# Performance work log

Hardware: AMD Instinct MI355X
Metric: run time of the kernel (lower is better)

## Reference

```python
import jax, jax.numpy as jnp
import numpy as np


def _gru_step(h, x, Wih, Whh, bih, bhh):
    # PyTorch GRU gate order: reset, update, new
    H = h.shape[-1]
    gx = x @ Wih.T + bih            # [B, 3H]
    gh = h @ Whh.T + bhh            # [B, 3H]
    r = jax.nn.sigmoid(gx[:, :H] + gh[:, :H])
    z = jax.nn.sigmoid(gx[:, H:2 * H] + gh[:, H:2 * H])
    n = jnp.tanh(gx[:, 2 * H:] + r * gh[:, 2 * H:])
    return (1.0 - z) * n + z * h


def setup_inputs() -> dict:
    key = jax.random.key(0)
    ks = jax.random.split(key, 20)
    B, S, L = 32, 200, 50
    Vt, Vs = 50000, 30000
    De, Ds, H = 256, 256, 512
    s = 0.05
    f = jnp.float32
    return {
        "method_code": jax.random.randint(ks[0], (B, S), 0, Vt),
        "method_summary": jax.random.randint(ks[1], (B, L), 0, Vs),
        "use_teacher": 1,
        "enc_emb": jax.random.normal(ks[2], (Vt, De), f) * s,
        "enc_Wih": jax.random.normal(ks[3], (3 * H, De), f) * s,
        "enc_Whh": jax.random.normal(ks[4], (3 * H, H), f) * s,
        "enc_bih": jax.random.normal(ks[5], (3 * H,), f) * s,
        "enc_bhh": jax.random.normal(ks[6], (3 * H,), f) * s,
        "dec_emb": jax.random.normal(ks[7], (Vs, Ds), f) * s,
        "dec_Wih": jax.random.normal(ks[8], (3 * H, Ds), f) * s,
        "dec_Whh": jax.random.normal(ks[9], (3 * H, H), f) * s,
        "dec_bih": jax.random.normal(ks[10], (3 * H,), f) * s,
        "dec_bhh": jax.random.normal(ks[11], (3 * H,), f) * s,
        "W1": jax.random.normal(ks[12], (H, 2 * H), f) * s,
        "b1": jax.random.normal(ks[13], (H,), f) * s,
        "W2": jax.random.normal(ks[14], (Vs, H), f) * s,
        "b2": jax.random.normal(ks[15], (Vs,), f) * s,
    }


def reference(method_code, method_summary, use_teacher,
              enc_emb, enc_Wih, enc_Whh, enc_bih, enc_bhh,
              dec_emb, dec_Wih, dec_Whh, dec_bih, dec_bhh,
              W1, b1, W2, b2):
    B = method_code.shape[0]
    H = enc_Whh.shape[1]
    # ---- GRU encoder over code tokens (hidden=None -> zeros) ----
    x_emb = enc_emb[method_code]                       # [B, S, De]
    h0 = jnp.zeros((B, H), x_emb.dtype)

    def enc_step(h, x):
        h = _gru_step(h, x, enc_Wih, enc_Whh, enc_bih, enc_bhh)
        return h, h

    h_last, enc_seq = jax.lax.scan(enc_step, h0, jnp.swapaxes(x_emb, 0, 1))
    enc_out = jnp.swapaxes(enc_seq, 0, 1)              # [B, S, H]

    # ---- attentive GRU decoder, teacher forcing (use_teacher=True) ----
    tokens = method_summary[:, :-1].T                  # [L-1, B]

    def dec_step(h, tok):
        emb = dec_emb[tok]                             # [B, Ds]
        h = _gru_step(h, emb, dec_Wih, dec_Whh, dec_bih, dec_bhh)
        attn = jax.nn.softmax(jnp.einsum('bh,bsh->bs', h, enc_out), axis=-1)
        ctx = jnp.einsum('bs,bsh->bh', attn, enc_out)  # [B, H]
        c = jnp.concatenate([ctx, h], axis=-1)         # [B, 2H]
        out = jax.nn.relu(c @ W1.T + b1) @ W2.T + b2   # [B, Vs]
        return h, out

    _, outs = jax.lax.scan(dec_step, h_last, tokens)   # [L-1, B, Vs]
    return jnp.swapaxes(outs, 0, 1)                    # [B, L-1, Vs]
```

## Files before the change

### kernel.cpp

```cpp
#include <hip/hip_runtime.h>
#include <cmath>

#define WGS  256
#define NWGR 256
#define DOMS 4
#define JGN  64
#define HBDW 5120

typedef float    f32x4 __attribute__((ext_vector_type(4)));
typedef unsigned u32x4 __attribute__((ext_vector_type(4)));
typedef short    s16x8 __attribute__((ext_vector_type(8)));
typedef unsigned short u16x4 __attribute__((ext_vector_type(4)));

#define B_   32
#define S_   200
#define L_   50
#define H_   512
#define DE_  256
#define VS_  30000
#define TD_  49
#define G3_  1536

#define OFF_ENC_GX  ((size_t)0)
#define SZ_ENC_GX   ((size_t)S_*B_*G3_)
#define OFF_DEC_GX  (OFF_ENC_GX + SZ_ENC_GX)
#define SZ_DEC_GX   ((size_t)TD_*B_*G3_)
#define OFF_ENC_OUT (OFF_DEC_GX + SZ_DEC_GX)
#define SZ_ENC_OUT  ((size_t)B_*S_*H_)
#define OFF_HBUF    (OFF_ENC_OUT + SZ_ENC_OUT)
#define SZ_HBUF     ((size_t)DOMS*2*HBDW)
#define OFF_CMAT    (OFF_HBUF + SZ_HBUF)
#define SZ_CMAT     ((size_t)TD_*B_*2*H_)
#define OFF_OUT1    (OFF_CMAT + SZ_CMAT)
#define SZ_OUT1     ((size_t)TD_*B_*H_)
#define OFF_W2HI    ((size_t)0)
#define OFF_W2LO    ((size_t)(VS_*H_/2))
#define OFF_O1HI    (OFF_OUT1 + SZ_OUT1)
#define OFF_O1LO    (OFF_O1HI + (size_t)(TD_*B_*H_/2))

#define RSTR 548
#define KBLK 68

__device__ __forceinline__ u32x4 load_u4_cc(const unsigned* p) {
  u32x4 v;
  asm volatile("global_load_dwordx4 %0, %1, off sc0 sc1" : "=v"(v) : "v"(p) : "memory");
  return v;
}

__device__ __forceinline__ float dot4(f32x4 a, f32x4 b) {
  return a.x * b.x + a.y * b.y + a.z * b.z + a.w * b.w;
}

__device__ __forceinline__ unsigned short f2bf(float f) {
  unsigned u = __float_as_uint(f);
  return (unsigned short)((u + 0x7fffu + ((u >> 16) & 1u)) >> 16);
}
__device__ __forceinline__ float bf2f(unsigned short h) {
  return __uint_as_float(((unsigned)h) << 16);
}

__global__ __launch_bounds__(WGS)
void recurrence_kernel(const float* __restrict__ enc_gx,
                       const float* __restrict__ dec_gx,
                       const float* __restrict__ eWhh, const float* __restrict__ eBhh,
                       const float* __restrict__ dWhh, const float* __restrict__ dBhh,
                       float* __restrict__ enc_out,
                       float* __restrict__ hbuf,
                       float* __restrict__ Cmat)
{
  __shared__ float hlds[8 * RSTR];
  __shared__ float red[768];

  const int t   = threadIdx.x;
  const int w   = blockIdx.x;
  const int dom = w >> 6;
  const int jg  = w & (JGN - 1);
  const int jl  = t & 7;
  const int kh  = t >> 3;
  const int bt_ = t >> 3;
  const int j   = (jg << 3) + jl;
  const int b_g = (dom << 3) + bt_;

  float* hdom = hbuf + (size_t)dom * (2 * HBDW);

  int rr[5], kb[5];
  #pragma unroll
  for (int i = 0; i < 5; ++i) {
    int g = i * 1024 + (t << 2);
    int blk = g / 80;
    rr[i] = g - blk * 80;
    kb[i] = blk << 3;
  }

  f32x4 wreg[3][4];
  auto load_w = [&](const float* __restrict__ W) {
    #pragma unroll
    for (int g = 0; g < 3; ++g)
      #pragma unroll
      for (int c = 0; c < 4; ++c)
        wreg[g][c] = *(const f32x4*)(W + (size_t)(g * H_ + j) * H_ + (kh << 4) + (c << 2));
  };
  load_w(eWhh);

  float bias_r = 0.f, bias_z = 0.f, bias_n = 0.f;
  if (t < 64) { bias_r = eBhh[j]; bias_z = eBhh[H_ + j]; bias_n = eBhh[2 * H_ + j]; }

  for (int s = 0; s < S_ + TD_; ++s) {
    const bool enc = (s < S_);
    __syncthreads();
    if (s == S_) {
      load_w(dWhh);
      if (t < 64) { bias_r = dBhh[j]; bias_z = dBhh[H_ + j]; bias_n = dBhh[2 * H_ + j]; }
    }

    float gxr = 0.f, gxz = 0.f, gxn = 0.f;
    if (t < 64) {
      const float* gx = enc ? (enc_gx + ((size_t)s * B_ + b_g) * G3_)
                            : (dec_gx + ((size_t)(s - S_) * B_ + b_g) * G3_);
      gxr = gx[j]; gxz = gx[H_ + j]; gxn = gx[2 * H_ + j];
    }

    {
      const unsigned* hb = (const unsigned*)(hdom + (size_t)(s & 1) * HBDW);
      const unsigned tagreq = (unsigned)s;
      u32x4 v0, v1, v2, v3, v4;
      while (true) {
        v0 = load_u4_cc(hb + 0 * 1024 + (t << 2));
        v1 = load_u4_cc(hb + 1 * 1024 + (t << 2));
        v2 = load_u4_cc(hb + 2 * 1024 + (t << 2));
        v3 = load_u4_cc(hb + 3 * 1024 + (t << 2));
        v4 = load_u4_cc(hb + 4 * 1024 + (t << 2));
        asm volatile("s_waitcnt vmcnt(0)" ::: "memory");
        bool ok = true;
        if ((rr[0] & 15) == 0) ok &= ((unsigned)v0.x >= tagreq);
        if ((rr[1] & 15) == 0) ok &= ((unsigned)v1.x >= tagreq);
        if ((rr[2] & 15) == 0) ok &= ((unsigned)v2.x >= tagreq);
        if ((rr[3] & 15) == 0) ok &= ((unsigned)v3.x >= tagreq);
        if ((rr[4] & 15) == 0) ok &= ((unsigned)v4.x >= tagreq);
        if (__all(ok)) break;
        __builtin_amdgcn_s_sleep(1);
      }
      #define SCAT(vv, ii) { \
        _Pragma("unroll") \
        for (int d = 0; d < 4; ++d) { \
          int pos = rr[ii] + d; \
          if ((pos & 15) != 0) { \
            int p = pos - 1 - (pos >> 4); \
            if (p < 64) { \
              int bb = p >> 3, k = kb[ii] + (p & 7); \
              hlds[bb * RSTR + ((k >> 6) * KBLK) + (k & 63)] = __uint_as_float(vv[d]); \
            } } } }
      SCAT(v0, 0) SCAT(v1, 1) SCAT(v2, 2) SCAT(v3, 3) SCAT(v4, 4)
      #undef SCAT
    }
    __syncthreads();

    float acc[3][8];
    #pragma unroll
    for (int g = 0; g < 3; ++g)
      #pragma unroll
      for (int b = 0; b < 8; ++b) acc[g][b] = 0.f;

    const int hoff = (kh >> 2) * KBLK + ((kh & 3) << 4);
    #pragma unroll
    for (int b = 0; b < 8; ++b) {
      const float* hp = &hlds[b * RSTR + hoff];
      f32x4 h0 = *(const f32x4*)(hp);
      f32x4 h1 = *(const f32x4*)(hp + 4);
      f32x4 h2 = *(const f32x4*)(hp + 8);
      f32x4 h3 = *(const f32x4*)(hp + 12);
      #pragma unroll
      for (int g = 0; g < 3; ++g)
        acc[g][b] += dot4(wreg[g][0], h0) + dot4(wreg[g][1], h1)
                   + dot4(wreg[g][2], h2) + dot4(wreg[g][3], h3);
    }

    #pragma unroll
    for (int g = 0; g < 3; ++g)
      #pragma unroll
      for (int b = 0; b < 8; ++b) {
        float v = acc[g][b];
        v += __shfl_xor(v, 8);
        v += __shfl_xor(v, 16);
        v += __shfl_xor(v, 32);
        acc[g][b] = v;
      }
    if ((t & 56) == 0) {
      const int base = ((t >> 6) * 8 + jl) * 24;
      #pragma unroll
      for (int g = 0; g < 3; ++g)
        #pragma unroll
        for (int b = 0; b < 8; ++b)
          red[base + g * 8 + b] = acc[g][b];
    }
    __syncthreads();

    if (t < 64) {
      float ar = 0.f, az = 0.f, an = 0.f;
      #pragma unroll
      for (int ww = 0; ww < 4; ++ww) {
        const int base = (ww * 8 + jl) * 24;
        ar += red[base + bt_];
        az += red[base + 8 + bt_];
        an += red[base + 16 + bt_];
      }
      float rg = 1.f / (1.f + expf(-(gxr + ar + bias_r)));
      float zg = 1.f / (1.f + expf(-(gxz + az + bias_z)));
      float ng = tanhf(gxn + rg * (an + bias_n));
      float hprev = hlds[bt_ * RSTR + ((j >> 6) * KBLK) + (j & 63)];
      float hn = (1.f - zg) * ng + zg * hprev;
      if (enc) enc_out[((size_t)b_g * S_ + s) * H_ + j] = hn;
      else     Cmat[((size_t)(s - S_) * B_ + b_g) * (2 * H_) + H_ + j] = hn;

      unsigned* pb = (unsigned*)(hdom + (size_t)((s + 1) & 1) * HBDW) + jg * 80;
      const unsigned tagv = (unsigned)(s + 1);
      float vA = __shfl(hn, (t - 1 - (t >> 4)) & 63);
      unsigned valA = ((t & 15) == 0) ? tagv : __float_as_uint(vA);
      __hip_atomic_store(pb + t, valA, __ATOMIC_RELAXED, __HIP_MEMORY_SCOPE_AGENT);
      float vB = __shfl(hn, (59 + t) & 63);
      if (t < 16) {
        unsigned valB = (t == 0) ? tagv : __float_as_uint(vB);
        __hip_atomic_store(pb + 64 + t, valB, __ATOMIC_RELAXED, __HIP_MEMORY_SCOPE_AGENT);
      }
    }
  }
}

__global__ __launch_bounds__(WGS)
void attention_kernel(const float* __restrict__ enc_out,
                      float* __restrict__ Cmat)
{
  const int task = blockIdx.x;
  const int td = task >> 5, b = task & 31;
  const int t = threadIdx.x;
  const float* h = Cmat + ((size_t)td * B_ + b) * (2 * H_) + H_;

  __shared__ float red[WGS];
  __shared__ float p[WGS];

  float sv = -1e30f;
  if (t < S_) {
    const float* eo = enc_out + ((size_t)b * S_ + t) * H_;
    float acc = 0.f;
    #pragma unroll 4
    for (int k = 0; k < H_; k += 4) {
      float4 e = *(const float4*)(eo + k);
      float4 hv = *(const float4*)(h + k);
      acc += e.x * hv.x + e.y * hv.y + e.z * hv.z + e.w * hv.w;
    }
    sv = acc;
  }
  red[t] = sv; __syncthreads();
  for (int o = 128; o; o >>= 1) { if (t < o) red[t] = fmaxf(red[t], red[t + o]); __syncthreads(); }
  float mx = red[0]; __syncthreads();
  float ev = (t < S_) ? expf(sv - mx) : 0.f;
  red[t] = ev; __syncthreads();
  for (int o = 128; o; o >>= 1) { if (t < o) red[t] += red[t + o]; __syncthreads(); }
  float inv = 1.f / red[0];
  p[t] = ev * inv;
  __syncthreads();

  const float* eo = enc_out + (size_t)b * S_ * H_ + (t << 1);
  float ax = 0.f, ay = 0.f;
  for (int i = 0; i < S_; ++i) {
    float pi = p[i];
    float2 v = *(const float2*)(eo + (size_t)i * H_);
    ax += pi * v.x; ay += pi * v.y;
  }
  float* cd = Cmat + ((size_t)td * B_ + b) * (2 * H_) + (t << 1);
  cd[0] = ax; cd[1] = ay;
}

template<int MODE>
__launch_bounds__(WGS)
__global__ void gemm128g(const float* __restrict__ A,
                         const int* __restrict__ idx,
                         const float* __restrict__ Bw,
                         const float* __restrict__ bias,
                         float* __restrict__ Cdst,
                         unsigned short* __restrict__ Ohi,
                         unsigned short* __restrict__ Olo,
                         int M, int N, int K)
{
  const int APAD = 132;
  __shared__ float As[16 * APAD];
  __shared__ float Bs[16 * APAD];
  __shared__ int toks[128];
  const int n0 = blockIdx.x * 128, m0 = blockIdx.y * 128;
  const int t = threadIdx.x;
  const int tx = t & 15, ty = t >> 4;

  if (MODE <= 1) {
    if (t < 128) {
      int m = m0 + t;
      int tok = 0;
      if (m < M) {
        int bidx = m & 31, sr = m >> 5;
        tok = (MODE == 0) ? idx[bidx * S_ + sr] : idx[bidx * L_ + sr];
      }
      toks[t] = tok;
    }
    __syncthreads();
  }

  float acc[8][8];
  #pragma unroll
  for (int i = 0; i < 8; ++i)
    #pragma unroll
    for (int jj = 0; jj < 8; ++jj) acc[i][jj] = 0.f;

  const int srow = t >> 2, skk = (t & 3) * 4;
  for (int k0 = 0; k0 < K; k0 += 16) {
    #pragma unroll
    for (int u = 0; u < 2; ++u) {
      int row = srow + u * 64;
      const float* asrc;
      if (MODE <= 1) {
        asrc = A + (size_t)toks[row] * K + k0 + skk;
      } else {
        int m = m0 + row; if (m >= M) m = M - 1;
        asrc = A + (size_t)m * K + k0 + skk;
      }
      f32x4 av = *(const f32x4*)asrc;
      As[(skk + 0) * APAD + row] = av.x;
      As[(skk + 1) * APAD + row] = av.y;
      As[(skk + 2) * APAD + row] = av.z;
      As[(skk + 3) * APAD + row] = av.w;
      int n = n0 + row;
      f32x4 bv = *(const f32x4*)(Bw + (size_t)n * K + k0 + skk);
      Bs[(skk + 0) * APAD + row] = bv.x;
      Bs[(skk + 1) * APAD + row] = bv.y;
      Bs[(skk + 2) * APAD + row] = bv.z;
      Bs[(skk + 3) * APAD + row] = bv.w;
    }
    __syncthreads();
    #pragma unroll
    for (int k = 0; k < 16; ++k) {
      f32x4 a0 = *(const f32x4*)&As[k * APAD + ty * 8];
      f32x4 a1 = *(const f32x4*)&As[k * APAD + ty * 8 + 4];
      f32x4 b0 = *(const f32x4*)&Bs[k * APAD + tx * 4];
      f32x4 b1 = *(const f32x4*)&Bs[k * APAD + 64 + tx * 4];
      float a[8] = {a0.x, a0.y, a0.z, a0.w, a1.x, a1.y, a1.z, a1.w};
      float bb[8] = {b0.x, b0.y, b0.z, b0.w, b1.x, b1.y, b1.z, b1.w};
      #pragma unroll
      for (int i = 0; i < 8; ++i)
        #pragma unroll
        for (int jj = 0; jj < 8; ++jj)
          acc[i][jj] += a[i] * bb[jj];
    }
    __syncthreads();
  }

  if (MODE <= 1) {
    f32x4 bias0 = *(const f32x4*)(bias + n0 + tx * 4);
    f32x4 bias1 = *(const f32x4*)(bias + n0 + 64 + tx * 4);
    #pragma unroll
    for (int i = 0; i < 8; ++i) {
      int m = m0 + ty * 8 + i;
      if (m >= M) continue;
      float* orow = Cdst + (size_t)m * N;
      f32x4 v0 = { acc[i][0] + bias0.x, acc[i][1] + bias0.y,
                   acc[i][2] + bias0.z, acc[i][3] + bias0.w };
      f32x4 v1 = { acc[i][4] + bias1.x, acc[i][5] + bias1.y,
                   acc[i][6] + bias1.z, acc[i][7] + bias1.w };
      *(f32x4*)(orow + n0 + tx * 4) = v0;
      *(f32x4*)(orow + n0 + 64 + tx * 4) = v1;
    }
  } else {
    #pragma unroll
    for (int i = 0; i < 8; ++i) {
      int m = m0 + ty * 8 + i;
      if (m >= M) continue;
      #pragma unroll
      for (int half = 0; half < 2; ++half) {
        u16x4 hv, lv;
        #pragma unroll
        for (int d = 0; d < 4; ++d) {
          int n = n0 + half * 64 + tx * 4 + d;
          float v = fmaxf(acc[i][half * 4 + d] + bias[n], 0.f);
          unsigned short hb = f2bf(v);
          hv[d] = hb;
          lv[d] = f2bf(v - bf2f(hb));
        }
        size_t o = (size_t)m * H_ + n0 + half * 64 + tx * 4;
        *(u16x4*)(Ohi + o) = hv;
        *(u16x4*)(Olo + o) = lv;
      }
    }
  }
}

__global__ __launch_bounds__(WGS)
void cvt_split(const float* __restrict__ x, unsigned short* __restrict__ hi,
               unsigned short* __restrict__ lo, int n4)
{
  int i = blockIdx.x * WGS + threadIdx.x;
  if (i >= n4) return;
  f32x4 v = *(const f32x4*)(x + (size_t)i * 4);
  u16x4 h, l;
  #pragma unroll
  for (int d = 0; d < 4; ++d) {
    unsigned short hb = f2bf(v[d]);
    h[d] = hb;
    l[d] = f2bf(v[d] - bf2f(hb));
  }
  *(u16x4*)(hi + (size_t)i * 4) = h;
  *(u16x4*)(lo + (size_t)i * 4) = l;
}

__global__ __launch_bounds__(WGS)
void gemm_mfma_out(const unsigned short* __restrict__ Ahi,
                   const unsigned short* __restrict__ Alo,
                   const unsigned short* __restrict__ Bhi,
                   const unsigned short* __restrict__ Blo,
                   const float* __restrict__ bias,
                   float* __restrict__ out)
{
  __shared__ char smem[65536];
  const int t = threadIdx.x;
  const int l = t & 63;
  const int wv = t >> 6;
  const int r = l & 15, q = l >> 4;
  const int m0 = blockIdx.x * 128;
  const int n0 = blockIdx.y * 128;
  const int M = TD_ * B_, N = VS_, K = H_;
  const int wm = (wv >> 1) << 6;
  const int wn = (wv & 1) << 6;

  int swoff[2];
  size_t aoff[2], boff[2];
  #pragma unroll
  for (int qq = 0; qq < 2; ++qq) {
    int chunk = qq * 256 + t;
    int row = chunk >> 2, c = chunk & 3;
    swoff[qq] = row * 64 + ((c ^ ((row >> 1) & 3)) << 4);
    int gm = m0 + row; if (gm >= M) gm = M - 1;
    aoff[qq] = (size_t)gm * K + c * 8;
    int gn = n0 + row; if (gn >= N) gn = N - 1;
    boff[qq] = (size_t)gn * K + c * 8;
  }

  u32x4 rg[8];
  auto gload = [&](int k0) {
    #pragma unroll
    for (int qq = 0; qq < 2; ++qq) {
      rg[qq]     = *(const u32x4*)(Ahi + aoff[qq] + k0);
      rg[2 + qq] = *(const u32x4*)(Alo + aoff[qq] + k0);
      rg[4 + qq] = *(const u32x4*)(Bhi + boff[qq] + k0);
      rg[6 + qq] = *(const u32x4*)(Blo + boff[qq] + k0);
    }
  };
  auto swrite = [&](char* buf) {
    #pragma unroll
    for (int qq = 0; qq < 2; ++qq) {
      *(u32x4*)(buf +         swoff[qq]) = rg[qq];
      *(u32x4*)(buf +  8192 + swoff[qq]) = rg[2 + qq];
      *(u32x4*)(buf + 16384 + swoff[qq]) = rg[4 + qq];
      *(u32x4*)(buf + 24576 + swoff[qq]) = rg[6 + qq];
    }
  };

  int afo[4], bfo[4];
  #pragma unroll
  for (int fi = 0; fi < 4; ++fi) {
    int ra = wm + fi * 16 + r;
    afo[fi] = ra * 64 + ((q ^ ((ra >> 1) & 3)) << 4);
    int rb = wn + fi * 16 + r;
    bfo[fi] = rb * 64 + ((q ^ ((rb >> 1) & 3)) << 4);
  }

  f32x4 acc[4][4];
  #pragma unroll
  for (int fi = 0; fi < 4; ++fi)
    #pragma unroll
    for (int nj = 0; nj < 4; ++nj) acc[fi][nj] = (f32x4){0.f, 0.f, 0.f, 0.f};

  gload(0);
  swrite(smem);
  __syncthreads();
  int cur = 0;
  const int NS = K / 32;
  for (int s = 0; s < NS; ++s) {
    if (s + 1 < NS) gload((s + 1) * 32);
    char* buf = smem + cur * 32768;
    s16x8 ah[4], al[4], bh[4], bl[4];
    #pragma unroll
    for (int fi = 0; fi < 4; ++fi) {
      ah[fi] = *(const s16x8*)(buf +         afo[fi]);
      al[fi] = *(const s16x8*)(buf +  8192 + afo[fi]);
      bh[fi] = *(const s16x8*)(buf + 16384 + bfo[fi]);
      bl[fi] = *(const s16x8*)(buf + 24576 + bfo[fi]);
    }
    #pragma unroll
    for (int fi = 0; fi < 4; ++fi)
      #pragma unroll
      for (int nj = 0; nj < 4; ++nj) {
        acc[fi][nj] = __builtin_amdgcn_mfma_f32_16x16x32_bf16(ah[fi], bh[nj], acc[fi][nj], 0, 0, 0);
        acc[fi][nj] = __builtin_amdgcn_mfma_f32_16x16x32_bf16(ah[fi], bl[nj], acc[fi][nj], 0, 0, 0);
        acc[fi][nj] = __builtin_amdgcn_mfma_f32_16x16x32_bf16(al[fi], bh[nj], acc[fi][nj], 0, 0, 0);
      }
    if (s + 1 < NS) swrite(smem + (cur ^ 1) * 32768);
    __syncthreads();
    cur ^= 1;
  }

  #pragma unroll
  for (int nj = 0; nj < 4; ++nj) {
    int n = n0 + wn + nj * 16 + r;
    if (n >= N) continue;
    float bv = bias[n];
    #pragma unroll
    for (int fi = 0; fi < 4; ++fi) {
      #pragma unroll
      for (int e = 0; e < 4; ++e) {
        int m = m0 + wm + fi * 16 + q * 4 + e;
        if (m < M) {
          int bidx = m & 31, td = m >> 5;
          out[((size_t)bidx * TD_ + td) * (size_t)N + n] = acc[fi][nj][e] + bv;
        }
      }
    }
  }
}

extern "C" void kernel_launch(void* const* d_in, const int* in_sizes, int n_in,
                              void* d_out, int out_size, void* d_ws, size_t ws_size,
                              hipStream_t stream) {
  const int*   method_code    = (const int*)d_in[0];
  const int*   method_summary = (const int*)d_in[1];
  const float* enc_emb = (const float*)d_in[3];
  const float* enc_Wih = (const float*)d_in[4];
  const float* enc_Whh = (const float*)d_in[5];
  const float* enc_bih = (const float*)d_in[6];
  const float* enc_bhh = (const float*)d_in[7];
  const float* dec_emb = (const float*)d_in[8];
  const float* dec_Wih = (const float*)d_in[9];
  const float* dec_Whh = (const float*)d_in[10];
  const float* dec_bih = (const float*)d_in[11];
  const float* dec_bhh = (const float*)d_in[12];
  const float* W1 = (const float*)d_in[13];
  const float* b1 = (const float*)d_in[14];
  const float* W2 = (const float*)d_in[15];
  const float* b2 = (const float*)d_in[16];

  float* ws      = (float*)d_ws;
  float* enc_gx  = ws + OFF_ENC_GX;
  float* dec_gx  = ws + OFF_DEC_GX;
  float* enc_out = ws + OFF_ENC_OUT;
  float* hbuf    = ws + OFF_HBUF;
  float* Cmat    = ws + OFF_CMAT;
  unsigned short* W2hi = (unsigned short*)(ws + OFF_W2HI);
  unsigned short* W2lo = (unsigned short*)(ws + OFF_W2LO);
  unsigned short* O1hi = (unsigned short*)(ws + OFF_O1HI);
  unsigned short* O1lo = (unsigned short*)(ws + OFF_O1LO);

  hipMemsetAsync(hbuf, 0, SZ_HBUF * sizeof(float), stream);

  dim3 blk(WGS);
  gemm128g<0><<<dim3(G3_ / 128, (S_ * B_) / 128), blk, 0, stream>>>(
      enc_emb, method_code, enc_Wih, enc_bih, enc_gx, nullptr, nullptr,
      S_ * B_, G3_, DE_);
  gemm128g<1><<<dim3(G3_ / 128, (TD_ * B_ + 127) / 128), blk, 0, stream>>>(
      dec_emb, method_summary, dec_Wih, dec_bih, dec_gx, nullptr, nullptr,
      TD_ * B_, G3_, DE_);

  recurrence_kernel<<<NWGR, blk, 0, stream>>>(enc_gx, dec_gx,
                                              enc_Whh, enc_bhh, dec_Whh, dec_bhh,
                                              enc_out, hbuf, Cmat);

  attention_kernel<<<TD_ * B_, blk, 0, stream>>>(enc_out, Cmat);

  cvt_split<<<(VS_ * H_ / 4 + WGS - 1) / WGS, blk, 0, stream>>>(
      W2, W2hi, W2lo, VS_ * H_ / 4);

  gemm128g<2><<<dim3(H_ / 128, (TD_ * B_ + 127) / 128), blk, 0, stream>>>(
      Cmat, nullptr, W1, b1, nullptr, O1hi, O1lo, TD_ * B_, H_, 2 * H_);

  gemm_mfma_out<<<dim3((TD_ * B_ + 127) / 128, (VS_ + 127) / 128), blk, 0, stream>>>(
      O1hi, O1lo, W2hi, W2lo, b2, (float*)d_out);
}
```

Baseline: 1.561 ms.

## Fuse input-gate projection into persistent GRU recurrence kernel with 8 batch domains

Removes the two separate input-projection GEMM launches and computes x·Wih inside the persistent recurrence kernel, gathering embeddings per step into LDS and holding Wih slices in registers. The work decomposition changes from 4 domains of 8 batches × 64 groups of 8 hidden units to 8 domains of 4 batches × 32 groups of 16 units, so each domain's hidden-state exchange buffer is smaller. The goal is to drop the gate-precompute kernels and their large gx round-trip through memory. The cost is more per-step arithmetic and register pressure on the serial critical path, plus an embedding gather at every step.

```diff
diff --git a/kernel.cpp b/kernel.cpp
--- a/kernel.cpp
+++ b/kernel.cpp
@@ -3,9 +3,9 @@
 
 #define WGS  256
 #define NWGR 256
-#define DOMS 4
-#define JGN  64
-#define HBDW 5120
+#define DOMS 8
+#define JGN  32
+#define HBDW 2560
 
 typedef float    f32x4 __attribute__((ext_vector_type(4)));
 typedef unsigned u32x4 __attribute__((ext_vector_type(4)));
@@ -21,11 +21,7 @@
 #define TD_  49
 #define G3_  1536
 
-#define OFF_ENC_GX  ((size_t)0)
-#define SZ_ENC_GX   ((size_t)S_*B_*G3_)
-#define OFF_DEC_GX  (OFF_ENC_GX + SZ_ENC_GX)
-#define SZ_DEC_GX   ((size_t)TD_*B_*G3_)
-#define OFF_ENC_OUT (OFF_DEC_GX + SZ_DEC_GX)
+#define OFF_ENC_OUT ((size_t)(S_*B_*G3_) + (size_t)(TD_*B_*G3_))
 #define SZ_ENC_OUT  ((size_t)B_*S_*H_)
 #define OFF_HBUF    (OFF_ENC_OUT + SZ_ENC_OUT)
 #define SZ_HBUF     ((size_t)DOMS*2*HBDW)
@@ -60,83 +56,101 @@
 }
 
 __global__ __launch_bounds__(WGS)
-void recurrence_kernel(const float* __restrict__ enc_gx,
-                       const float* __restrict__ dec_gx,
+void recurrence_kernel(const int* __restrict__ mc, const int* __restrict__ ms,
+                       const float* __restrict__ enc_emb,
+                       const float* __restrict__ eWih, const float* __restrict__ eBih,
+                       const float* __restrict__ dec_emb,
+                       const float* __restrict__ dWih, const float* __restrict__ dBih,
                        const float* __restrict__ eWhh, const float* __restrict__ eBhh,
                        const float* __restrict__ dWhh, const float* __restrict__ dBhh,
                        float* __restrict__ enc_out,
                        float* __restrict__ hbuf,
                        float* __restrict__ Cmat)
 {
-  __shared__ float hlds[8 * RSTR];
+  __shared__ float hlds[4 * RSTR];
+  __shared__ float xlds[4 * 256];
   __shared__ float red[768];
+  __shared__ float red2[768];
 
   const int t   = threadIdx.x;
   const int w   = blockIdx.x;
-  const int dom = w >> 6;
+  const int dom = w >> 5;
   const int jg  = w & (JGN - 1);
-  const int jl  = t & 7;
-  const int kh  = t >> 3;
-  const int bt_ = t >> 3;
-  const int j   = (jg << 3) + jl;
-  const int b_g = (dom << 3) + bt_;
+  const int kh  = t >> 4;
+  const int j   = (jg << 4) + (t & 15);
+  const int bt_ = t >> 4;
+  const int b_g = (dom << 2) + bt_;
+  const int xb  = t >> 6, xc = t & 63;
+  const int xb_g = (dom << 2) + xb;
 
   float* hdom = hbuf + (size_t)dom * (2 * HBDW);
 
-  int rr[5], kb[5];
-  #pragma unroll
-  for (int i = 0; i < 5; ++i) {
+  int rr[3], kb[3];
+  #pragma unroll
+  for (int i = 0; i < 3; ++i) {
     int g = i * 1024 + (t << 2);
     int blk = g / 80;
     rr[i] = g - blk * 80;
-    kb[i] = blk << 3;
-  }
-
-  f32x4 wreg[3][4];
-  auto load_w = [&](const float* __restrict__ W) {
+    kb[i] = blk << 4;
+  }
+
+  f32x4 whh[3][8];
+  auto load_whh = [&](const float* __restrict__ W) {
     #pragma unroll
     for (int g = 0; g < 3; ++g)
       #pragma unroll
+      for (int c = 0; c < 8; ++c)
+        whh[g][c] = *(const f32x4*)(W + (size_t)(g * H_ + j) * H_ + (kh << 5) + (c << 2));
+  };
+  f32x4 wih[3][4];
+  auto load_wih = [&](const float* __restrict__ W) {
+    #pragma unroll
+    for (int g = 0; g < 3; ++g)
+      #pragma unroll
       for (int c = 0; c < 4; ++c)
-        wreg[g][c] = *(const f32x4*)(W + (size_t)(g * H_ + j) * H_ + (kh << 4) + (c << 2));
+        wih[g][c] = *(const f32x4*)(W + (size_t)(g * H_ + j) * DE_ + (kh << 4) + (c << 2));
   };
-  load_w(eWhh);
-
-  float bias_r = 0.f, bias_z = 0.f, bias_n = 0.f;
-  if (t < 64) { bias_r = eBhh[j]; bias_z = eBhh[H_ + j]; bias_n = eBhh[2 * H_ + j]; }
+  load_whh(eWhh);
+  load_wih(eWih);
+
+  float bhr = 0.f, bhz = 0.f, bhn = 0.f, bxr = 0.f, bxz = 0.f, bxn = 0.f;
+  if (t < 64) {
+    bhr = eBhh[j]; bhz = eBhh[H_ + j]; bhn = eBhh[2 * H_ + j];
+    bxr = eBih[j]; bxz = eBih[H_ + j]; bxn = eBih[2 * H_ + j];
+  }
 
   for (int s = 0; s < S_ + TD_; ++s) {
     const bool enc = (s < S_);
     __syncthreads();
     if (s == S_) {
-      load_w(dWhh);
-      if (t < 64) { bias_r = dBhh[j]; bias_z = dBhh[H_ + j]; bias_n = dBhh[2 * H_ + j]; }
-    }
-
-    float gxr = 0.f, gxz = 0.f, gxn = 0.f;
-    if (t < 64) {
-      const float* gx = enc ? (enc_gx + ((size_t)s * B_ + b_g) * G3_)
-                            : (dec_gx + ((size_t)(s - S_) * B_ + b_g) * G3_);
-      gxr = gx[j]; gxz = gx[H_ + j]; gxn = gx[2 * H_ + j];
+      load_whh(dWhh);
+      load_wih(dWih);
+      if (t < 64) {
+        bhr = dBhh[j]; bhz = dBhh[H_ + j]; bhn = dBhh[2 * H_ + j];
+        bxr = dBih[j]; bxz = dBih[H_ + j]; bxn = dBih[2 * H_ + j];
+      }
+    }
+
+    {
+      int tok = enc ? mc[xb_g * S_ + s] : ms[xb_g * L_ + (s - S_)];
+      const float* emb = enc ? enc_emb : dec_emb;
+      f32x4 xv = *(const f32x4*)(emb + (size_t)tok * DE_ + (xc << 2));
+      *(f32x4*)&xlds[xb * 256 + (xc << 2)] = xv;
     }
 
     {
       const unsigned* hb = (const unsigned*)(hdom + (size_t)(s & 1) * HBDW);
       const unsigned tagreq = (unsigned)s;
-      u32x4 v0, v1, v2, v3, v4;
+      u32x4 v0, v1, v2;
       while (true) {
         v0 = load_u4_cc(hb + 0 * 1024 + (t << 2));
         v1 = load_u4_cc(hb + 1 * 1024 + (t << 2));
-        v2 = load_u4_cc(hb + 2 * 1024 + (t << 2));
-        v3 = load_u4_cc(hb + 3 * 1024 + (t << 2));
-        v4 = load_u4_cc(hb + 4 * 1024 + (t << 2));
+        if (t < 128) v2 = load_u4_cc(hb + 2 * 1024 + (t << 2));
         asm volatile("s_waitcnt vmcnt(0)" ::: "memory");
         bool ok = true;
         if ((rr[0] & 15) == 0) ok &= ((unsigned)v0.x >= tagreq);
         if ((rr[1] & 15) == 0) ok &= ((unsigned)v1.x >= tagreq);
-        if ((rr[2] & 15) == 0) ok &= ((unsigned)v2.x >= tagreq);
-        if ((rr[3] & 15) == 0) ok &= ((unsigned)v3.x >= tagreq);
-        if ((rr[4] & 15) == 0) ok &= ((unsigned)v4.x >= tagreq);
+        if (t < 128 && (rr[2] & 15) == 0) ok &= ((unsigned)v2.x >= tagreq);
         if (__all(ok)) break;
         __builtin_amdgcn_s_sleep(1);
       }
@@ -147,66 +161,77 @@
           if ((pos & 15) != 0) { \
             int p = pos - 1 - (pos >> 4); \
             if (p < 64) { \
-              int bb = p >> 3, k = kb[ii] + (p & 7); \
+              int bb = p >> 4, k = kb[ii] + (p & 15); \
               hlds[bb * RSTR + ((k >> 6) * KBLK) + (k & 63)] = __uint_as_float(vv[d]); \
             } } } }
-      SCAT(v0, 0) SCAT(v1, 1) SCAT(v2, 2) SCAT(v3, 3) SCAT(v4, 4)
+      SCAT(v0, 0) SCAT(v1, 1)
+      if (t < 128) { SCAT(v2, 2) }
       #undef SCAT
     }
     __syncthreads();
 
-    float acc[3][8];
+    float acc[3][4], acx[3][4];
     #pragma unroll
     for (int g = 0; g < 3; ++g)
       #pragma unroll
-      for (int b = 0; b < 8; ++b) acc[g][b] = 0.f;
-
-    const int hoff = (kh >> 2) * KBLK + ((kh & 3) << 4);
-    #pragma unroll
-    for (int b = 0; b < 8; ++b) {
+      for (int b = 0; b < 4; ++b) { acc[g][b] = 0.f; acx[g][b] = 0.f; }
+
+    const int hoff = (kh >> 1) * KBLK + (kh & 1) * 32;
+    #pragma unroll
+    for (int b = 0; b < 4; ++b) {
       const float* hp = &hlds[b * RSTR + hoff];
-      f32x4 h0 = *(const f32x4*)(hp);
-      f32x4 h1 = *(const f32x4*)(hp + 4);
-      f32x4 h2 = *(const f32x4*)(hp + 8);
-      f32x4 h3 = *(const f32x4*)(hp + 12);
-      #pragma unroll
-      for (int g = 0; g < 3; ++g)
-        acc[g][b] += dot4(wreg[g][0], h0) + dot4(wreg[g][1], h1)
-                   + dot4(wreg[g][2], h2) + dot4(wreg[g][3], h3);
+      #pragma unroll
+      for (int c = 0; c < 8; ++c) {
+        f32x4 hv = *(const f32x4*)(hp + (c << 2));
+        acc[0][b] += dot4(whh[0][c], hv);
+        acc[1][b] += dot4(whh[1][c], hv);
+        acc[2][b] += dot4(whh[2][c], hv);
+      }
+      const float* xp = &xlds[b * 256 + (kh << 4)];
+      #pragma unroll
+      for (int c = 0; c < 4; ++c) {
+        f32x4 xv = *(const f32x4*)(xp + (c << 2));
+        acx[0][b] += dot4(wih[0][c], xv);
+        acx[1][b] += dot4(wih[1][c], xv);
+        acx[2][b] += dot4(wih[2][c], xv);
+      }
     }
 
     #pragma unroll
     for (int g = 0; g < 3; ++g)
       #pragma unroll
-      for (int b = 0; b < 8; ++b) {
+      for (int b = 0; b < 4; ++b) {
         float v = acc[g][b];
-        v += __shfl_xor(v, 8);
-        v += __shfl_xor(v, 16);
-        v += __shfl_xor(v, 32);
+        v += __shfl_xor(v, 16); v += __shfl_xor(v, 32);
         acc[g][b] = v;
-      }
-    if ((t & 56) == 0) {
-      const int base = ((t >> 6) * 8 + jl) * 24;
+        float u = acx[g][b];
+        u += __shfl_xor(u, 16); u += __shfl_xor(u, 32);
+        acx[g][b] = u;
+      }
+    if ((t & 48) == 0) {
+      const int base = (t >> 6) * 192 + (t & 15) * 12;
       #pragma unroll
       for (int g = 0; g < 3; ++g)
         #pragma unroll
-        for (int b = 0; b < 8; ++b)
-          red[base + g * 8 + b] = acc[g][b];
+        for (int b = 0; b < 4; ++b) {
+          red[base + g * 4 + b]  = acc[g][b];
+          red2[base + g * 4 + b] = acx[g][b];
+        }
     }
     __syncthreads();
 
     if (t < 64) {
-      float ar = 0.f, az = 0.f, an = 0.f;
+      float ar = 0.f, az = 0.f, an = 0.f, xr = 0.f, xz = 0.f, xn = 0.f;
       #pragma unroll
       for (int ww = 0; ww < 4; ++ww) {
-        const int base = (ww * 8 + jl) * 24;
-        ar += red[base + bt_];
-        az += red[base + 8 + bt_];
-        an += red[base + 16 + bt_];
-      }
-      float rg = 1.f / (1.f + expf(-(gxr + ar + bias_r)));
-      float zg = 1.f / (1.f + expf(-(gxz + az + bias_z)));
-      float ng = tanhf(gxn + rg * (an + bias_n));
+        const int base = ww * 192 + (t & 15) * 12 + bt_;
+        ar += red[base];      az += red[base + 4];  an += red[base + 8];
+        xr += red2[base];     xz += red2[base + 4]; xn += red2[base + 8];
+      }
+      float gxr = xr + bxr, gxz = xz + bxz, gxn = xn + bxn;
+      float rg = 1.f / (1.f + expf(-(gxr + ar + bhr)));
+      float zg = 1.f / (1.f + expf(-(gxz + az + bhz)));
+      float ng = tanhf(gxn + rg * (an + bhn));
       float hprev = hlds[bt_ * RSTR + ((j >> 6) * KBLK) + (j & 63)];
       float hn = (1.f - zg) * ng + zg * hprev;
       if (enc) enc_out[((size_t)b_g * S_ + s) * H_ + j] = hn;
@@ -271,38 +296,21 @@
   cd[0] = ax; cd[1] = ay;
 }
 
-template<int MODE>
 __launch_bounds__(WGS)
-__global__ void gemm128g(const float* __restrict__ A,
-                         const int* __restrict__ idx,
-                         const float* __restrict__ Bw,
-                         const float* __restrict__ bias,
-                         float* __restrict__ Cdst,
-                         unsigned short* __restrict__ Ohi,
-                         unsigned short* __restrict__ Olo,
-                         int M, int N, int K)
+__global__ void gemm128_fc1(const float* __restrict__ A,
+                            const float* __restrict__ Bw,
+                            const float* __restrict__ bias,
+                            unsigned short* __restrict__ Ohi,
+                            unsigned short* __restrict__ Olo,
+                            int M, int N, int K)
 {
   const int APAD = 132;
   __shared__ float As[16 * APAD];
   __shared__ float Bs[16 * APAD];
-  __shared__ int toks[128];
   const int n0 = blockIdx.x * 128, m0 = blockIdx.y * 128;
   const int t = threadIdx.x;
   const int tx = t & 15, ty = t >> 4;
 
-  if (MODE <= 1) {
-    if (t < 128) {
-      int m = m0 + t;
-      int tok = 0;
-      if (m < M) {
-        int bidx = m & 31, sr = m >> 5;
-        tok = (MODE == 0) ? idx[bidx * S_ + sr] : idx[bidx * L_ + sr];
-      }
-      toks[t] = tok;
-    }
-    __syncthreads();
-  }
-
   float acc[8][8];
   #pragma unroll
   for (int i = 0; i < 8; ++i)
@@ -314,14 +322,8 @@
     #pragma unroll
     for (int u = 0; u < 2; ++u) {
       int row = srow + u * 64;
-      const float* asrc;
-      if (MODE <= 1) {
-        asrc = A + (size_t)toks[row] * K + k0 + skk;
-      } else {
-        int m = m0 + row; if (m >= M) m = M - 1;
-        asrc = A + (size_t)m * K + k0 + skk;
-      }
-      f32x4 av = *(const f32x4*)asrc;
+      int m = m0 + row; if (m >= M) m = M - 1;
+      f32x4 av = *(const f32x4*)(A + (size_t)m * K + k0 + skk);
       As[(skk + 0) * APAD + row] = av.x;
       As[(skk + 1) * APAD + row] = av.y;
       As[(skk + 2) * APAD + row] = av.z;
@@ -351,41 +353,24 @@
     __syncthreads();
   }
 
-  if (MODE <= 1) {
-    f32x4 bias0 = *(const f32x4*)(bias + n0 + tx * 4);
-    f32x4 bias1 = *(const f32x4*)(bias + n0 + 64 + tx * 4);
-    #pragma unroll
-    for (int i = 0; i < 8; ++i) {
-      int m = m0 + ty * 8 + i;
-      if (m >= M) continue;
-      float* orow = Cdst + (size_t)m * N;
-      f32x4 v0 = { acc[i][0] + bias0.x, acc[i][1] + bias0.y,
-                   acc[i][2] + bias0.z, acc[i][3] + bias0.w };
-      f32x4 v1 = { acc[i][4] + bias1.x, acc[i][5] + bias1.y,
-                   acc[i][6] + bias1.z, acc[i][7] + bias1.w };
-      *(f32x4*)(orow + n0 + tx * 4) = v0;
-      *(f32x4*)(orow + n0 + 64 + tx * 4) = v1;
-    }
-  } else {
-    #pragma unroll
-    for (int i = 0; i < 8; ++i) {
-      int m = m0 + ty * 8 + i;
-      if (m >= M) continue;
-      #pragma unroll
-      for (int half = 0; half < 2; ++half) {
-        u16x4 hv, lv;
-        #pragma unroll
-        for (int d = 0; d < 4; ++d) {
-          int n = n0 + half * 64 + tx * 4 + d;
-          float v = fmaxf(acc[i][half * 4 + d] + bias[n], 0.f);
-          unsigned short hb = f2bf(v);
-          hv[d] = hb;
-          lv[d] = f2bf(v - bf2f(hb));
-        }
-        size_t o = (size_t)m * H_ + n0 + half * 64 + tx * 4;
-        *(u16x4*)(Ohi + o) = hv;
-        *(u16x4*)(Olo + o) = lv;
-      }
+  #pragma unroll
+  for (int i = 0; i < 8; ++i) {
+    int m = m0 + ty * 8 + i;
+    if (m >= M) continue;
+    #pragma unroll
+    for (int half = 0; half < 2; ++half) {
+      u16x4 hv, lv;
+      #pragma unroll
+      for (int d = 0; d < 4; ++d) {
+        int n = n0 + half * 64 + tx * 4 + d;
+        float v = fmaxf(acc[i][half * 4 + d] + bias[n], 0.f);
+        unsigned short hb = f2bf(v);
+        hv[d] = hb;
+        lv[d] = f2bf(v - bf2f(hb));
+      }
+      size_t o = (size_t)m * H_ + n0 + half * 64 + tx * 4;
+      *(u16x4*)(Ohi + o) = hv;
+      *(u16x4*)(Olo + o) = lv;
     }
   }
 }
@@ -544,8 +529,6 @@
   const float* b2 = (const float*)d_in[16];
 
   float* ws      = (float*)d_ws;
-  float* enc_gx  = ws + OFF_ENC_GX;
-  float* dec_gx  = ws + OFF_DEC_GX;
   float* enc_out = ws + OFF_ENC_OUT;
   float* hbuf    = ws + OFF_HBUF;
   float* Cmat    = ws + OFF_CMAT;
@@ -557,24 +540,21 @@
   hipMemsetAsync(hbuf, 0, SZ_HBUF * sizeof(float), stream);
 
   dim3 blk(WGS);
-  gemm128g<0><<<dim3(G3_ / 128, (S_ * B_) / 128), blk, 0, stream>>>(
-      enc_emb, method_code, enc_Wih, enc_bih, enc_gx, nullptr, nullptr,
-      S_ * B_, G3_, DE_);
-  gemm128g<1><<<dim3(G3_ / 128, (TD_ * B_ + 127) / 128), blk, 0, stream>>>(
-      dec_emb, method_summary, dec_Wih, dec_bih, dec_gx, nullptr, nullptr,
-      TD_ * B_, G3_, DE_);
-
-  recurrence_kernel<<<NWGR, blk, 0, stream>>>(enc_gx, dec_gx,
-                                              enc_Whh, enc_bhh, dec_Whh, dec_bhh,
-                                              enc_out, hbuf, Cmat);
+
+  recurrence_kernel<<<NWGR, blk, 0, stream>>>(
+      method_code, method_summary,
+      enc_emb, enc_Wih, enc_bih,
+      dec_emb, dec_Wih, dec_bih,
+      enc_Whh, enc_bhh, dec_Whh, dec_bhh,
+      enc_out, hbuf, Cmat);
 
   attention_kernel<<<TD_ * B_, blk, 0, stream>>>(enc_out, Cmat);
 
   cvt_split<<<(VS_ * H_ / 4 + WGS - 1) / WGS, blk, 0, stream>>>(
       W2, W2hi, W2lo, VS_ * H_ / 4);
 
-  gemm128g<2><<<dim3(H_ / 128, (TD_ * B_ + 127) / 128), blk, 0, stream>>>(
-      Cmat, nullptr, W1, b1, nullptr, O1hi, O1lo, TD_ * B_, H_, 2 * H_);
+  gemm128_fc1<<<dim3(H_ / 128, (TD_ * B_ + 127) / 128), blk, 0, stream>>>(
+      Cmat, W1, b1, O1hi, O1lo, TD_ * B_, H_, 2 * H_);
 
   gemm_mfma_out<<<dim3((TD_ * B_ + 127) / 128, (VS_ + 127) / 128), blk, 0, stream>>>(
       O1hi, O1lo, W2hi, W2lo, b2, (float*)d_out);
```

After: 1.497 ms. -4.1%, faster.
